# Kernel tuning notes

Hardware: AMD Instinct MI355X
Metric: run time of the kernel (lower is better)

## Reference

```python
import math
import jax, jax.numpy as jnp
import numpy as np


def _gelu(x):
    return jax.nn.gelu(x, approximate=False)


def _bilinear_sample(feat, gx, gy):
    """grid_sample, mode=bilinear, padding=border, align_corners=True.
    feat: [B,C,H,W]; gx,gy: [B,M] in [-1,1]. Returns [B,M,C]."""
    B, C, H, W = feat.shape
    x = jnp.clip((gx + 1.0) * 0.5 * (W - 1), 0.0, W - 1)
    y = jnp.clip((gy + 1.0) * 0.5 * (H - 1), 0.0, H - 1)
    x0 = jnp.floor(x); y0 = jnp.floor(y)
    wx = (x - x0)[..., None]; wy = (y - y0)[..., None]
    x0i = x0.astype(jnp.int32); y0i = y0.astype(jnp.int32)
    x1i = jnp.minimum(x0i + 1, W - 1); y1i = jnp.minimum(y0i + 1, H - 1)
    ft = jnp.transpose(feat, (0, 2, 3, 1))  # [B,H,W,C]
    gather = jax.vmap(lambda f, yi, xi: f[yi, xi])
    v00 = gather(ft, y0i, x0i); v01 = gather(ft, y0i, x1i)
    v10 = gather(ft, y1i, x0i); v11 = gather(ft, y1i, x1i)
    return (v00 * (1 - wx) * (1 - wy) + v01 * wx * (1 - wy)
            + v10 * (1 - wx) * wy + v11 * wx * wy)


def _layernorm(x, w, b, eps=1e-5):
    m = jnp.mean(x, -1, keepdims=True)
    v = jnp.var(x, -1, keepdims=True)
    return (x - m) / jnp.sqrt(v + eps) * w + b


def _gfb(h, f_next, ph_w, ph_b, gate, w1, b1, w2, b2, ln_w, ln_b):
    g = jax.nn.sigmoid(gate)
    fused = f_next + g * (h @ ph_w + ph_b)
    fused = _gelu(fused @ w1 + b1) @ w2 + b2
    return _layernorm(fused, ln_w, ln_b)


def _forward(img, feat_s8, feat_s16, coarse_flow, query_coords,
             pp_w1, pp_b1, pp_w2, pp_b2, p8_w, p8_b, p16_w, p16_b,
             f1_ph_w, f1_ph_b, f1_gate, f1_w1, f1_b1, f1_w2, f1_b2, f1_ln_w, f1_ln_b,
             f2_ph_w, f2_ph_b, f2_gate, f2_w1, f2_b1, f2_w2, f2_b2, f2_ln_w, f2_ln_b,
             h_w1, h_b1, h_w2, h_b2, h_w3, h_b3):
    B, _, H, W = img.shape
    N = query_coords.shape[1]
    k = 5; half = k // 2
    H8, W8 = coarse_flow.shape[2], coarse_flow.shape[3]
    # normalized grid at query points (x,y)
    gx = 2.0 * query_coords[..., 0] / (W - 1) - 1.0
    gy = 2.0 * query_coords[..., 1] / (H - 1) - 1.0
    coarse_q = _bilinear_sample(coarse_flow, gx, gy)  # [B,N,2]
    coarse_q = coarse_q * jnp.array([W / W8, H / H8], coarse_q.dtype)
    # local k x k RGB patches
    offs = jnp.arange(-half, half + 1, dtype=img.dtype)
    oy, ox = jnp.meshgrid(offs, offs, indexing='ij')
    og = jnp.stack([ox.reshape(-1), oy.reshape(-1)], -1)  # [k*k,2]
    ce = query_coords[:, :, None, :] + og                # [B,N,kk,2]
    pgx = (2.0 * ce[..., 0] / (W - 1) - 1.0).reshape(B, -1)
    pgy = (2.0 * ce[..., 1] / (H - 1) - 1.0).reshape(B, -1)
    patches = _bilinear_sample(img, pgx, pgy).reshape(B, N, k * k * 3)
    f_local = _gelu(patches @ pp_w1 + pp_b1) @ pp_w2 + pp_b2
    f8 = _bilinear_sample(feat_s8, gx, gy) @ p8_w + p8_b
    f16 = _bilinear_sample(feat_s16, gx, gy) @ p16_w + p16_b
    D = f_local.shape[-1]
    h = f_local.reshape(B * N, D)
    h = _gfb(h, f8.reshape(B * N, D), f1_ph_w, f1_ph_b, f1_gate,
             f1_w1, f1_b1, f1_w2, f1_b2, f1_ln_w, f1_ln_b)
    h = _gfb(h, f16.reshape(B * N, D), f2_ph_w, f2_ph_b, f2_gate,
             f2_w1, f2_b1, f2_w2, f2_b2, f2_ln_w, f2_ln_b)
    # relative-in-cell coords + sinusoidal PE (6 bands)
    qx = query_coords[..., 0] / (W / W8)
    qy = query_coords[..., 1] / (H / H8)
    local = jnp.stack([(qx - jnp.round(qx)) * 2.0, (qy - jnp.round(qy)) * 2.0], -1)
    freqs = (2.0 ** jnp.arange(6, dtype=local.dtype)) * math.pi
    xf = local[..., None] * freqs                        # [B,N,2,6]
    enc = jnp.concatenate([jnp.sin(xf), jnp.cos(xf)], -1).reshape(B, N, 24)
    pe = jnp.concatenate([local, enc], -1).reshape(B * N, 26)
    coarse_flat = coarse_q.reshape(B * N, 2)
    mi = jnp.concatenate([h, pe, coarse_flat], -1)       # [B*N, 156]
    delta = _gelu(_gelu(mi @ h_w1 + h_b1) @ h_w2 + h_b2) @ h_w3 + h_b3
    return (coarse_flat + delta).reshape(B, N, 2)


def setup_inputs() -> dict:
    key = jax.random.key(0)
    ks = jax.random.split(key, 40)
    B, H, W = 2, 384, 512
    H8, W8, H16, W16 = 48, 64, 24, 32
    N, D, k = 65536, 128, 5
    pf = 3 * k * k
    def p(i, shape):
        return jax.random.normal(ks[i], shape, jnp.float32) * 0.05
    return {
        'img': jax.random.uniform(ks[0], (B, 3, H, W), jnp.float32),
        'feat_s8': jax.random.normal(ks[1], (B, D, H8, W8), jnp.float32),
        'feat_s16': jax.random.normal(ks[2], (B, D, H16, W16), jnp.float32),
        'coarse_flow': jax.random.normal(ks[3], (B, 2, H8, W8), jnp.float32),
        'query_coords': jax.random.uniform(ks[4], (B, N, 2), jnp.float32)
                        * jnp.array([W - 1.0, H - 1.0], jnp.float32),
        'pp_w1': p(5, (pf, D)), 'pp_b1': p(6, (D,)),
        'pp_w2': p(7, (D, D)), 'pp_b2': p(8, (D,)),
        'p8_w': p(9, (D, D)), 'p8_b': p(10, (D,)),
        'p16_w': p(11, (D, D)), 'p16_b': p(12, (D,)),
        'f1_ph_w': p(13, (D, D)), 'f1_ph_b': p(14, (D,)), 'f1_gate': p(15, (D,)),
        'f1_w1': p(16, (D, 2 * D)), 'f1_b1': p(17, (2 * D,)),
        'f1_w2': p(18, (2 * D, D)), 'f1_b2': p(19, (D,)),
        'f1_ln_w': 1.0 + p(20, (D,)), 'f1_ln_b': p(21, (D,)),
        'f2_ph_w': p(22, (D, D)), 'f2_ph_b': p(23, (D,)), 'f2_gate': p(24, (D,)),
        'f2_w1': p(25, (D, 2 * D)), 'f2_b1': p(26, (2 * D,)),
        'f2_w2': p(27, (2 * D, D)), 'f2_b2': p(28, (D,)),
        'f2_ln_w': 1.0 + p(29, (D,)), 'f2_ln_b': p(30, (D,)),
        'h_w1': p(31, (D + 26 + 2, 128)), 'h_b1': p(32, (128,)),
        'h_w2': p(33, (128, 64)), 'h_b2': p(34, (64,)),
        'h_w3': p(35, (64, 2)), 'h_b3': p(36, (2,)),
    }


def reference(img, feat_s8, feat_s16, coarse_flow, query_coords,
              pp_w1, pp_b1, pp_w2, pp_b2, p8_w, p8_b, p16_w, p16_b,
              f1_ph_w, f1_ph_b, f1_gate, f1_w1, f1_b1, f1_w2, f1_b2, f1_ln_w, f1_ln_b,
              f2_ph_w, f2_ph_b, f2_gate, f2_w1, f2_b1, f2_w2, f2_b2, f2_ln_w, f2_ln_b,
              h_w1, h_b1, h_w2, h_b2, h_w3, h_b3):
    return _forward(img, feat_s8, feat_s16, coarse_flow, query_coords,
                    pp_w1, pp_b1, pp_w2, pp_b2, p8_w, p8_b, p16_w, p16_b,
                    f1_ph_w, f1_ph_b, f1_gate, f1_w1, f1_b1, f1_w2, f1_b2, f1_ln_w, f1_ln_b,
                    f2_ph_w, f2_ph_b, f2_gate, f2_w1, f2_b1, f2_w2, f2_b2, f2_ln_w, f2_ln_b,
                    h_w1, h_b1, h_w2, h_b2, h_w3, h_b3)
```

## Files before the change

kernel.cpp:

```cpp
#include <hip/hip_runtime.h>
#include <math.h>

#define NT 512
#define MB 64
#define MTOT 131072
#define IMG_H 384
#define IMG_W 512
#define H8 48
#define W8 64
#define H16 24
#define W16 32

#define SAB 136
#define SHB 168

typedef _Float16 half8_t __attribute__((ext_vector_type(8)));
typedef _Float16 half4_t __attribute__((ext_vector_type(4)));
typedef float f32x4_t __attribute__((ext_vector_type(4)));
typedef unsigned short u16;

#define PW_PP1    0
#define PW_PP2    12288
#define PW_P8CAT  28672
#define PW_P16CAT 61440
#define PW_F1W1   94208
#define PW_F1W2   126976
#define PW_F2W1   159744
#define PW_F2W2   192512
#define PW_HW1    225280
#define PW_HW2    245760
#define PW_END    253952
#define FT8_OFF   PW_END
#define FT8_CNT   (2*H8*W8*128)
#define FT16_OFF  (FT8_OFF + FT8_CNT)
#define FT16_CNT  (2*H16*W16*128)
#define FB_OFF    (FT16_OFF + FT16_CNT)

__device__ __forceinline__ u16 tohalf(float v) {
  return __builtin_bit_cast(u16, (_Float16)v);
}
__device__ __forceinline__ float geluf(float x) {
  float x2 = x * x;
  float t = x * fmaf(x2, 0.0713548162726f, 1.5957691216057308f);
  float e = __expf(-t);
  return x * __builtin_amdgcn_rcpf(1.0f + e);
}

__device__ __forceinline__ float bilin_plane(const float* __restrict__ plane,
                                             int Wd, int Hd, float x, float y) {
  x = fminf(fmaxf(x, 0.f), (float)(Wd - 1));
  y = fminf(fmaxf(y, 0.f), (float)(Hd - 1));
  float x0f = floorf(x), y0f = floorf(y);
  int x0 = (int)x0f, y0 = (int)y0f;
  int x1 = min(x0 + 1, Wd - 1), y1 = min(y0 + 1, Hd - 1);
  float wx = x - x0f, wy = y - y0f;
  const float* r0 = plane + y0 * Wd;
  const float* r1 = plane + y1 * Wd;
  float v00 = r0[x0], v01 = r0[x1], v10 = r1[x0], v11 = r1[x1];
  float top = v00 + wx * (v01 - v00);
  float bot = v10 + wx * (v11 - v10);
  return top + wy * (bot - top);
}

__device__ __forceinline__ void featSample(const u16* __restrict__ ft, int Wd, int Hd,
                                           float x, float y, u16* dstRow, int i16) {
  x = fminf(fmaxf(x, 0.f), (float)(Wd - 1));
  y = fminf(fmaxf(y, 0.f), (float)(Hd - 1));
  float x0f = floorf(x), y0f = floorf(y);
  int x0 = (int)x0f, y0 = (int)y0f;
  int x1 = min(x0 + 1, Wd - 1), y1 = min(y0 + 1, Hd - 1);
  float wx = x - x0f, wy = y - y0f;
  half8_t v00 = *reinterpret_cast<const half8_t*>(ft + (y0 * Wd + x0) * 128 + i16 * 8);
  half8_t v01 = *reinterpret_cast<const half8_t*>(ft + (y0 * Wd + x1) * 128 + i16 * 8);
  half8_t v10 = *reinterpret_cast<const half8_t*>(ft + (y1 * Wd + x0) * 128 + i16 * 8);
  half8_t v11 = *reinterpret_cast<const half8_t*>(ft + (y1 * Wd + x1) * 128 + i16 * 8);
  half8_t r;
#pragma unroll
  for (int j = 0; j < 8; ++j) {
    float top = (float)v00[j] + wx * ((float)v01[j] - (float)v00[j]);
    float bot = (float)v10[j] + wx * ((float)v11[j] - (float)v10[j]);
    r[j] = (_Float16)(top + wy * (bot - top));
  }
  *reinterpret_cast<half8_t*>(dstRow + i16 * 8) = r;
}

template <int NTW, int KT, int SPLITKT, int ACT, int NWAVES = 8>
__device__ __forceinline__ void mmv(
    const u16* __restrict__ wpk,
    const u16* aA, int strA, const u16* aB, int strB,
    const float* __restrict__ bias,
    u16* oA, int ostrA, u16* oB, int ostrB, int oSplitNt) {
  const int tid = threadIdx.x;
  const int lane = tid & 63;
  const int w = tid >> 6;
  const int l15 = lane & 15;
  const int g = lane >> 4;
  if (NWAVES == 8 || w < NWAVES) {
    f32x4_t acc[NTW][4];
#pragma unroll
    for (int i = 0; i < NTW; ++i)
#pragma unroll
      for (int mt = 0; mt < 4; ++mt) acc[i][mt] = (f32x4_t){0.f, 0.f, 0.f, 0.f};
#pragma unroll
    for (int kt = 0; kt < KT; ++kt) {
      const u16* ab = (kt < SPLITKT) ? (aA + kt * 32) : (aB + (kt - SPLITKT) * 32);
      const int str = (kt < SPLITKT) ? strA : strB;
      half8_t af[4];
#pragma unroll
      for (int mt = 0; mt < 4; ++mt)
        af[mt] = *reinterpret_cast<const half8_t*>(ab + (mt * 16 + l15) * str + g * 8);
#pragma unroll
      for (int i = 0; i < NTW; ++i) {
        const int nt = w + (i << 3);
        half8_t bf = *reinterpret_cast<const half8_t*>(wpk + ((nt * KT + kt) * 64 + lane) * 8);
#pragma unroll
        for (int mt = 0; mt < 4; ++mt)
          acc[i][mt] = __builtin_amdgcn_mfma_f32_16x16x32_f16(bf, af[mt], acc[i][mt], 0, 0, 0);
      }
    }
#pragma unroll
    for (int i = 0; i < NTW; ++i) {
      const int nt = w + (i << 3);
      const int colg = nt << 4;
      f32x4_t bv = *reinterpret_cast<const f32x4_t*>(bias + colg + (g << 2));
      u16* ob; int colB, ostr;
      if (nt < oSplitNt) { ob = oA; colB = colg; ostr = ostrA; }
      else { ob = oB; colB = colg - (oSplitNt << 4); ostr = ostrB; }
#pragma unroll
      for (int mt = 0; mt < 4; ++mt) {
        const int row = (mt << 4) + l15;
        half4_t hv;
#pragma unroll
        for (int r = 0; r < 4; ++r) {
          float v = acc[i][mt][r] + bv[r];
          if (ACT == 1) v = geluf(v);
          hv[r] = (_Float16)v;
        }
        *reinterpret_cast<half4_t*>(ob + row * ostr + colB + (g << 2)) = hv;
      }
    }
  }
}

__device__ __forceinline__ void lnorm(const u16* src, u16* dst,
                                      const float* __restrict__ lw,
                                      const float* __restrict__ lb) {
  const int tid = threadIdx.x;
  int q = tid >> 3, s = tid & 7;
  const u16* rp = src + q * SAB + s * 16;
  float xs[16];
  float sum = 0.f, sum2 = 0.f;
#pragma unroll
  for (int c8 = 0; c8 < 2; ++c8) {
    half8_t v = *reinterpret_cast<const half8_t*>(rp + c8 * 8);
#pragma unroll
    for (int j = 0; j < 8; ++j) {
      float x = (float)v[j];
      xs[c8 * 8 + j] = x; sum += x; sum2 += x * x;
    }
  }
  sum += __shfl_xor(sum, 1); sum2 += __shfl_xor(sum2, 1);
  sum += __shfl_xor(sum, 2); sum2 += __shfl_xor(sum2, 2);
  sum += __shfl_xor(sum, 4); sum2 += __shfl_xor(sum2, 4);
  float mean = sum * 0.0078125f;
  float var = sum2 * 0.0078125f - mean * mean;
  float rstd = rsqrtf(var + 1e-5f);
  u16* op = dst + q * SHB + s * 16;
#pragma unroll
  for (int c8 = 0; c8 < 2; ++c8) {
    half8_t r;
#pragma unroll
    for (int j = 0; j < 8; ++j) {
      int c = s * 16 + c8 * 8 + j;
      r[j] = (_Float16)((xs[c8 * 8 + j] - mean) * rstd * lw[c] + lb[c]);
    }
    *reinterpret_cast<half8_t*>(op + c8 * 8) = r;
  }
}

struct PackArgs {
  const float *pp_w1, *pp_w2, *p8_w, *f1_ph_w, *f1_gate, *p16_w, *f2_ph_w, *f2_gate;
  const float *f1_w1, *f1_w2, *f2_w1, *f2_w2, *h_w1, *h_w2;
  u16* dst;
};

__global__ void pack_weights(PackArgs a) {
  const int KTs[10]   = {3, 4, 8, 8, 4, 8, 4, 8, 5, 4};
  const int Ks[10]    = {75, 128, 256, 256, 128, 256, 128, 256, 156, 128};
  const int bases[11] = {0, 12288, 28672, 61440, 94208, 126976,
                         159744, 192512, 225280, 245760, 253952};
  int stride = gridDim.x * blockDim.x;
  for (int i = blockIdx.x * blockDim.x + threadIdx.x; i < PW_END; i += stride) {
    int s = 0;
    while (i >= bases[s + 1]) ++s;
    int rem = i - bases[s];
    int e = rem & 511, lane = e >> 3, j = e & 7;
    int ntkt = rem >> 9;
    int kt = ntkt % KTs[s], nt = ntkt / KTs[s];
    int k = kt * 32 + ((lane >> 4) << 3) + j;
    int col = (nt << 4) + (lane & 15);
    float v = 0.f;
    if (k < Ks[s]) {
      switch (s) {
        case 0: v = a.pp_w1[k * 128 + col]; break;
        case 1: v = a.pp_w2[k * 128 + col]; break;
        case 2: v = (k < 128) ? a.p8_w[k * 128 + col]
                              : a.f1_ph_w[(k - 128) * 128 + col] /
                                    (1.f + expf(-a.f1_gate[col])); break;
        case 3: v = (k < 128) ? a.p16_w[k * 128 + col]
                              : a.f2_ph_w[(k - 128) * 128 + col] /
                                    (1.f + expf(-a.f2_gate[col])); break;
        case 4: v = a.f1_w1[k * 256 + col]; break;
        case 5: v = a.f1_w2[k * 128 + col]; break;
        case 6: v = a.f2_w1[k * 256 + col]; break;
        case 7: v = a.f2_w2[k * 128 + col]; break;
        case 8: v = a.h_w1[k * 128 + col]; break;
        case 9: v = a.h_w2[k * 64 + col]; break;
      }
    }
    a.dst[i] = tohalf(v);
  }
}

__global__ void fuse_bias(const float* __restrict__ p8_b, const float* __restrict__ f1_ph_b,
                          const float* __restrict__ f1_gate,
                          const float* __restrict__ p16_b, const float* __restrict__ f2_ph_b,
                          const float* __restrict__ f2_gate, float* __restrict__ fb) {
  int t = threadIdx.x;
  if (t < 128) {
    fb[t] = p8_b[t] + f1_ph_b[t] / (1.f + expf(-f1_gate[t]));
    fb[128 + t] = p16_b[t] + f2_ph_b[t] / (1.f + expf(-f2_gate[t]));
  }
}

__global__ void cvt_cl_f16(const float* __restrict__ src, u16* __restrict__ dst,
                           int Hd, int Wd) {
  int total = 2 * 128 * Hd * Wd;
  int stride = gridDim.x * blockDim.x;
  for (int i = blockIdx.x * blockDim.x + threadIdx.x; i < total; i += stride) {
    int x = i % Wd;
    int t = i / Wd;
    int y = t % Hd; t /= Hd;
    int c = t % 128;
    int b = t / 128;
    dst[((b * Hd + y) * Wd + x) * 128 + c] = tohalf(src[i]);
  }
}

struct KParams {
  const float *img, *coarse_flow, *qc;
  const u16 *wpk, *ft8, *ft16;
  const float *fb;
  const float *pp_b1, *pp_b2;
  const float *f1_b1, *f1_b2, *f1_ln_w, *f1_ln_b;
  const float *f2_b1, *f2_b2, *f2_ln_w, *f2_ln_b;
  const float *h_b1, *h_b2, *h_w3, *h_b3;
  float* out;
};

__global__ __launch_bounds__(NT, 2) void ifd_mfma(KParams P) {
  __shared__ __align__(16) u16 smem[2 * (MB * SAB) + MB * SHB];
  __shared__ float qcL[2 * MB];
  __shared__ float cb[2 * MB];
  u16* ab0 = smem;
  u16* ab1 = smem + MB * SAB;
  u16* hb  = smem + 2 * MB * SAB;

  const int tid = threadIdx.x;
  const int m0 = blockIdx.x * MB;

  if (tid < 2 * MB) qcL[tid] = P.qc[m0 * 2 + tid];
  __syncthreads();

  for (int i = tid; i < MB * 96; i += NT) {
    int q = i / 96, c = i - q * 96;
    u16 val = 0;
    if (c < 75) {
      int m = m0 + q, b = m >> 16;
      float qx = qcL[2 * q], qy = qcL[2 * q + 1];
      int p = c / 3, ch = c - p * 3;
      int iy = p / 5, ix = p - iy * 5;
      const float* plane = P.img + (b * 3 + ch) * (IMG_H * IMG_W);
      val = tohalf(bilin_plane(plane, IMG_W, IMG_H,
                               qx + (float)(ix - 2), qy + (float)(iy - 2)));
    }
    ab0[q * SAB + c] = val;
  }
  for (int i = tid; i < MB * 40; i += NT) {
    int q = i / 40, c = i - q * 40;
    int m = m0 + q, b = m >> 16;
    float qx = qcL[2 * q], qy = qcL[2 * q + 1];
    float val = 0.f;
    if (c < 26) {
      float qx8 = qx * 0.125f, qy8 = qy * 0.125f;
      float lx = (qx8 - rintf(qx8)) * 2.f, ly = (qy8 - rintf(qy8)) * 2.f;
      if (c < 2) val = c ? ly : lx;
      else {
        int k = c - 2;
        int dim = k / 12, tt = k - dim * 12;
        int band = tt % 6, iscos = tt / 6;
        float loc = dim ? ly : lx;
        float ang = loc * 3.14159265358979323846f * (float)(1 << band);
        val = iscos ? __cosf(ang) : __sinf(ang);
      }
    } else if (c < 28) {
      int o = c - 26;
      float x8 = qx * (63.f / 511.f), y8 = qy * (47.f / 383.f);
      float cv = 8.f * bilin_plane(P.coarse_flow + (b * 2 + o) * (H8 * W8), W8, H8, x8, y8);
      cb[q * 2 + o] = cv;
      val = cv;
    }
    hb[q * SHB + 128 + c] = tohalf(val);
  }
  __syncthreads();

  mmv<1, 3, 3, 1>(P.wpk + PW_PP1, ab0, SAB, ab0, SAB, P.pp_b1,
                  ab1, SAB, ab1, SAB, 16);
  __syncthreads();
  mmv<1, 4, 4, 0>(P.wpk + PW_PP2, ab1, SAB, ab1, SAB, P.pp_b2,
                  hb, SHB, hb, SHB, 16);
  for (int i = tid; i < MB * 16; i += NT) {
    int q = i >> 4, i16 = i & 15;
    int m = m0 + q, b = m >> 16;
    float x = qcL[2 * q] * (63.f / 511.f), y = qcL[2 * q + 1] * (47.f / 383.f);
    featSample(P.ft8 + b * (H8 * W8 * 128), W8, H8, x, y, ab0 + q * SAB, i16);
  }
  __syncthreads();
  mmv<1, 8, 4, 0>(P.wpk + PW_P8CAT, ab0, SAB, hb, SHB, P.fb,
                  ab1, SAB, ab1, SAB, 16);
  __syncthreads();
  mmv<2, 4, 4, 1>(P.wpk + PW_F1W1, ab1, SAB, ab1, SAB, P.f1_b1,
                  ab0, SAB, hb, SHB, 8);
  __syncthreads();
  mmv<1, 8, 4, 0>(P.wpk + PW_F1W2, ab0, SAB, hb, SHB, P.f1_b2,
                  ab1, SAB, ab1, SAB, 16);
  __syncthreads();
  lnorm(ab1, hb, P.f1_ln_w, P.f1_ln_b);
  for (int i = tid; i < MB * 16; i += NT) {
    int q = i >> 4, i16 = i & 15;
    int m = m0 + q, b = m >> 16;
    float x = qcL[2 * q] * (31.f / 511.f), y = qcL[2 * q + 1] * (23.f / 383.f);
    featSample(P.ft16 + b * (H16 * W16 * 128), W16, H16, x, y, ab0 + q * SAB, i16);
  }
  __syncthreads();
  mmv<1, 8, 4, 0>(P.wpk + PW_P16CAT, ab0, SAB, hb, SHB, P.fb + 128,
                  ab1, SAB, ab1, SAB, 16);
  __syncthreads();
  mmv<2, 4, 4, 1>(P.wpk + PW_F2W1, ab1, SAB, ab1, SAB, P.f2_b1,
                  ab0, SAB, hb, SHB, 8);
  __syncthreads();
  mmv<1, 8, 4, 0>(P.wpk + PW_F2W2, ab0, SAB, hb, SHB, P.f2_b2,
                  ab1, SAB, ab1, SAB, 16);
  __syncthreads();
  lnorm(ab1, hb, P.f2_ln_w, P.f2_ln_b);
  __syncthreads();
  mmv<1, 5, 5, 1>(P.wpk + PW_HW1, hb, SHB, hb, SHB, P.h_b1,
                  ab1, SAB, ab1, SAB, 16);
  __syncthreads();
  mmv<1, 4, 4, 1, 4>(P.wpk + PW_HW2, ab1, SAB, ab1, SAB, P.h_b2,
                     ab0, SAB, ab0, SAB, 16);
  __syncthreads();
  if (tid < 2 * MB) {
    int q = tid >> 1, o = tid & 1;
    float acc = P.h_b3[o];
    const u16* rp = ab0 + q * SAB;
#pragma unroll
    for (int c8 = 0; c8 < 8; ++c8) {
      half8_t v = *reinterpret_cast<const half8_t*>(rp + c8 * 8);
#pragma unroll
      for (int j = 0; j < 8; ++j) acc += (float)v[j] * P.h_w3[(c8 * 8 + j) * 2 + o];
    }
    P.out[(m0 + q) * 2 + o] = cb[q * 2 + o] + acc;
  }
}

extern "C" void kernel_launch(void* const* d_in, const int* in_sizes, int n_in,
                              void* d_out, int out_size, void* d_ws, size_t ws_size,
                              hipStream_t stream) {
  u16* wp = (u16*)d_ws;
  float* fb = (float*)(wp + FB_OFF);

  PackArgs pa;
  pa.pp_w1  = (const float*)d_in[5];
  pa.pp_w2  = (const float*)d_in[7];
  pa.p8_w   = (const float*)d_in[9];
  pa.p16_w  = (const float*)d_in[11];
  pa.f1_ph_w = (const float*)d_in[13];
  pa.f1_gate = (const float*)d_in[15];
  pa.f1_w1  = (const float*)d_in[16];
  pa.f1_w2  = (const float*)d_in[18];
  pa.f2_ph_w = (const float*)d_in[22];
  pa.f2_gate = (const float*)d_in[24];
  pa.f2_w1  = (const float*)d_in[25];
  pa.f2_w2  = (const float*)d_in[27];
  pa.h_w1   = (const float*)d_in[31];
  pa.h_w2   = (const float*)d_in[33];
  pa.dst = wp;
  pack_weights<<<512, 256, 0, stream>>>(pa);
  fuse_bias<<<1, 128, 0, stream>>>((const float*)d_in[10], (const float*)d_in[14],
                                   (const float*)d_in[15], (const float*)d_in[12],
                                   (const float*)d_in[23], (const float*)d_in[24], fb);
  cvt_cl_f16<<<1024, 256, 0, stream>>>((const float*)d_in[1], wp + FT8_OFF, H8, W8);
  cvt_cl_f16<<<256, 256, 0, stream>>>((const float*)d_in[2], wp + FT16_OFF, H16, W16);

  KParams P;
  P.img = (const float*)d_in[0];
  P.coarse_flow = (const float*)d_in[3];
  P.qc = (const float*)d_in[4];
  P.wpk = wp; P.ft8 = wp + FT8_OFF; P.ft16 = wp + FT16_OFF;
  P.fb = fb;
  P.pp_b1 = (const float*)d_in[6];  P.pp_b2 = (const float*)d_in[8];
  P.f1_b1 = (const float*)d_in[17]; P.f1_b2 = (const float*)d_in[19];
  P.f1_ln_w = (const float*)d_in[20]; P.f1_ln_b = (const float*)d_in[21];
  P.f2_b1 = (const float*)d_in[26]; P.f2_b2 = (const float*)d_in[28];
  P.f2_ln_w = (const float*)d_in[29]; P.f2_ln_b = (const float*)d_in[30];
  P.h_b1 = (const float*)d_in[32]; P.h_b2 = (const float*)d_in[34];
  P.h_w3 = (const float*)d_in[35]; P.h_b3 = (const float*)d_in[36];
  P.out = (float*)d_out;

  ifd_mfma<<<MTOT / MB, NT, 0, stream>>>(P);
}
```

Before: 182.5 us.

## Prefetch next layer weights into registers during MFMA and raise occupancy

Each MLP layer's packed weight fragments are now loaded into registers by a callback that runs after the current layer's MFMA loop, before its epilogue, so global weight fetch latency overlaps with compute and the barrier. Launch bounds go from 2 to 4 blocks per CU, and query coordinates are read straight from global memory instead of being staged in shared memory with an extra barrier. The feature bilinear interpolation now uses packed fp16 vector math instead of fp32, which lowers precision. Holding prefetched fragments and the tighter register budget from the raised launch bound risk spills.

```diff
diff --git a/kernel.cpp b/kernel.cpp
--- a/kernel.cpp
+++ b/kernel.cpp
@@ -69,34 +69,48 @@
   float x0f = floorf(x), y0f = floorf(y);
   int x0 = (int)x0f, y0 = (int)y0f;
   int x1 = min(x0 + 1, Wd - 1), y1 = min(y0 + 1, Hd - 1);
-  float wx = x - x0f, wy = y - y0f;
+  _Float16 wx = (_Float16)(x - x0f), wy = (_Float16)(y - y0f);
   half8_t v00 = *reinterpret_cast<const half8_t*>(ft + (y0 * Wd + x0) * 128 + i16 * 8);
   half8_t v01 = *reinterpret_cast<const half8_t*>(ft + (y0 * Wd + x1) * 128 + i16 * 8);
   half8_t v10 = *reinterpret_cast<const half8_t*>(ft + (y1 * Wd + x0) * 128 + i16 * 8);
   half8_t v11 = *reinterpret_cast<const half8_t*>(ft + (y1 * Wd + x1) * 128 + i16 * 8);
-  half8_t r;
-#pragma unroll
-  for (int j = 0; j < 8; ++j) {
-    float top = (float)v00[j] + wx * ((float)v01[j] - (float)v00[j]);
-    float bot = (float)v10[j] + wx * ((float)v11[j] - (float)v10[j]);
-    r[j] = (_Float16)(top + wy * (bot - top));
-  }
+  half8_t top = v00 + wx * (v01 - v00);
+  half8_t bot = v10 + wx * (v11 - v10);
+  half8_t r = top + wy * (bot - top);
   *reinterpret_cast<half8_t*>(dstRow + i16 * 8) = r;
 }
 
-template <int NTW, int KT, int SPLITKT, int ACT, int NWAVES = 8>
+template <int NTW, int KT, int NWAVES = 8>
+__device__ __forceinline__ void wload(const u16* __restrict__ wpk, half8_t* bf) {
+  const int tid = threadIdx.x;
+  const int lane = tid & 63;
+  const int w = tid >> 6;
+  if (NWAVES == 8 || w < NWAVES) {
+#pragma unroll
+    for (int i = 0; i < NTW; ++i) {
+      const int nt = w + (i << 3);
+#pragma unroll
+      for (int kt = 0; kt < KT; ++kt)
+        bf[i * KT + kt] =
+            *reinterpret_cast<const half8_t*>(wpk + ((nt * KT + kt) * 64 + lane) * 8);
+    }
+  }
+}
+
+template <int NTW, int KT, int SPLITKT, int ACT, int NWAVES = 8, typename PF>
 __device__ __forceinline__ void mmv(
-    const u16* __restrict__ wpk,
+    const half8_t* __restrict__ bf,
     const u16* aA, int strA, const u16* aB, int strB,
     const float* __restrict__ bias,
-    u16* oA, int ostrA, u16* oB, int ostrB, int oSplitNt) {
+    u16* oA, int ostrA, u16* oB, int ostrB, int oSplitNt, PF&& pf) {
   const int tid = threadIdx.x;
   const int lane = tid & 63;
   const int w = tid >> 6;
   const int l15 = lane & 15;
   const int g = lane >> 4;
-  if (NWAVES == 8 || w < NWAVES) {
-    f32x4_t acc[NTW][4];
+  const bool active = (NWAVES == 8) || (w < NWAVES);
+  f32x4_t acc[NTW][4];
+  if (active) {
 #pragma unroll
     for (int i = 0; i < NTW; ++i)
 #pragma unroll
@@ -111,13 +125,15 @@
         af[mt] = *reinterpret_cast<const half8_t*>(ab + (mt * 16 + l15) * str + g * 8);
 #pragma unroll
       for (int i = 0; i < NTW; ++i) {
-        const int nt = w + (i << 3);
-        half8_t bf = *reinterpret_cast<const half8_t*>(wpk + ((nt * KT + kt) * 64 + lane) * 8);
 #pragma unroll
         for (int mt = 0; mt < 4; ++mt)
-          acc[i][mt] = __builtin_amdgcn_mfma_f32_16x16x32_f16(bf, af[mt], acc[i][mt], 0, 0, 0);
+          acc[i][mt] = __builtin_amdgcn_mfma_f32_16x16x32_f16(bf[i * KT + kt], af[mt],
+                                                              acc[i][mt], 0, 0, 0);
       }
     }
+  }
+  pf();
+  if (active) {
 #pragma unroll
     for (int i = 0; i < NTW; ++i) {
       const int nt = w + (i << 3);
@@ -258,9 +274,8 @@
   float* out;
 };
 
-__global__ __launch_bounds__(NT, 2) void ifd_mfma(KParams P) {
+__global__ __launch_bounds__(NT, 4) void ifd_mfma(KParams P) {
   __shared__ __align__(16) u16 smem[2 * (MB * SAB) + MB * SHB];
-  __shared__ float qcL[2 * MB];
   __shared__ float cb[2 * MB];
   u16* ab0 = smem;
   u16* ab1 = smem + MB * SAB;
@@ -269,15 +284,17 @@
   const int tid = threadIdx.x;
   const int m0 = blockIdx.x * MB;
 
-  if (tid < 2 * MB) qcL[tid] = P.qc[m0 * 2 + tid];
-  __syncthreads();
+  half8_t bS1[3], bS2[4], bS45[8], bS7[8], bS8[8], bS1112[8], bS14[8], bS15[8],
+      bS18[5], bS19[4];
+
+  wload<1, 3>(P.wpk + PW_PP1, bS1);
 
   for (int i = tid; i < MB * 96; i += NT) {
     int q = i / 96, c = i - q * 96;
     u16 val = 0;
     if (c < 75) {
       int m = m0 + q, b = m >> 16;
-      float qx = qcL[2 * q], qy = qcL[2 * q + 1];
+      float qx = P.qc[2 * m], qy = P.qc[2 * m + 1];
       int p = c / 3, ch = c - p * 3;
       int iy = p / 5, ix = p - iy * 5;
       const float* plane = P.img + (b * 3 + ch) * (IMG_H * IMG_W);
@@ -289,7 +306,7 @@
   for (int i = tid; i < MB * 40; i += NT) {
     int q = i / 40, c = i - q * 40;
     int m = m0 + q, b = m >> 16;
-    float qx = qcL[2 * q], qy = qcL[2 * q + 1];
+    float qx = P.qc[2 * m], qy = P.qc[2 * m + 1];
     float val = 0.f;
     if (c < 26) {
       float qx8 = qx * 0.125f, qy8 = qy * 0.125f;
@@ -314,51 +331,51 @@
   }
   __syncthreads();
 
-  mmv<1, 3, 3, 1>(P.wpk + PW_PP1, ab0, SAB, ab0, SAB, P.pp_b1,
-                  ab1, SAB, ab1, SAB, 16);
-  __syncthreads();
-  mmv<1, 4, 4, 0>(P.wpk + PW_PP2, ab1, SAB, ab1, SAB, P.pp_b2,
-                  hb, SHB, hb, SHB, 16);
+  mmv<1, 3, 3, 1>(bS1, ab0, SAB, ab0, SAB, P.pp_b1, ab1, SAB, ab1, SAB, 16,
+                  [&] { wload<1, 4>(P.wpk + PW_PP2, bS2); });
+  __syncthreads();
+  mmv<1, 4, 4, 0>(bS2, ab1, SAB, ab1, SAB, P.pp_b2, hb, SHB, hb, SHB, 16,
+                  [&] { wload<1, 8>(P.wpk + PW_P8CAT, bS45); });
   for (int i = tid; i < MB * 16; i += NT) {
     int q = i >> 4, i16 = i & 15;
     int m = m0 + q, b = m >> 16;
-    float x = qcL[2 * q] * (63.f / 511.f), y = qcL[2 * q + 1] * (47.f / 383.f);
+    float x = P.qc[2 * m] * (63.f / 511.f), y = P.qc[2 * m + 1] * (47.f / 383.f);
     featSample(P.ft8 + b * (H8 * W8 * 128), W8, H8, x, y, ab0 + q * SAB, i16);
   }
   __syncthreads();
-  mmv<1, 8, 4, 0>(P.wpk + PW_P8CAT, ab0, SAB, hb, SHB, P.fb,
-                  ab1, SAB, ab1, SAB, 16);
-  __syncthreads();
-  mmv<2, 4, 4, 1>(P.wpk + PW_F1W1, ab1, SAB, ab1, SAB, P.f1_b1,
-                  ab0, SAB, hb, SHB, 8);
-  __syncthreads();
-  mmv<1, 8, 4, 0>(P.wpk + PW_F1W2, ab0, SAB, hb, SHB, P.f1_b2,
-                  ab1, SAB, ab1, SAB, 16);
+  mmv<1, 8, 4, 0>(bS45, ab0, SAB, hb, SHB, P.fb, ab1, SAB, ab1, SAB, 16,
+                  [&] { wload<2, 4>(P.wpk + PW_F1W1, bS7); });
+  __syncthreads();
+  mmv<2, 4, 4, 1>(bS7, ab1, SAB, ab1, SAB, P.f1_b1, ab0, SAB, hb, SHB, 8,
+                  [&] { wload<1, 8>(P.wpk + PW_F1W2, bS8); });
+  __syncthreads();
+  mmv<1, 8, 4, 0>(bS8, ab0, SAB, hb, SHB, P.f1_b2, ab1, SAB, ab1, SAB, 16,
+                  [&] { wload<1, 8>(P.wpk + PW_P16CAT, bS1112); });
   __syncthreads();
   lnorm(ab1, hb, P.f1_ln_w, P.f1_ln_b);
   for (int i = tid; i < MB * 16; i += NT) {
     int q = i >> 4, i16 = i & 15;
     int m = m0 + q, b = m >> 16;
-    float x = qcL[2 * q] * (31.f / 511.f), y = qcL[2 * q + 1] * (23.f / 383.f);
+    float x = P.qc[2 * m] * (31.f / 511.f), y = P.qc[2 * m + 1] * (23.f / 383.f);
     featSample(P.ft16 + b * (H16 * W16 * 128), W16, H16, x, y, ab0 + q * SAB, i16);
   }
   __syncthreads();
-  mmv<1, 8, 4, 0>(P.wpk + PW_P16CAT, ab0, SAB, hb, SHB, P.fb + 128,
-                  ab1, SAB, ab1, SAB, 16);
-  __syncthreads();
-  mmv<2, 4, 4, 1>(P.wpk + PW_F2W1, ab1, SAB, ab1, SAB, P.f2_b1,
-                  ab0, SAB, hb, SHB, 8);
-  __syncthreads();
-  mmv<1, 8, 4, 0>(P.wpk + PW_F2W2, ab0, SAB, hb, SHB, P.f2_b2,
-                  ab1, SAB, ab1, SAB, 16);
+  mmv<1, 8, 4, 0>(bS1112, ab0, SAB, hb, SHB, P.fb + 128, ab1, SAB, ab1, SAB, 16,
+                  [&] { wload<2, 4>(P.wpk + PW_F2W1, bS14); });
+  __syncthreads();
+  mmv<2, 4, 4, 1>(bS14, ab1, SAB, ab1, SAB, P.f2_b1, ab0, SAB, hb, SHB, 8,
+                  [&] { wload<1, 8>(P.wpk + PW_F2W2, bS15); });
+  __syncthreads();
+  mmv<1, 8, 4, 0>(bS15, ab0, SAB, hb, SHB, P.f2_b2, ab1, SAB, ab1, SAB, 16,
+                  [&] { wload<1, 5>(P.wpk + PW_HW1, bS18); });
   __syncthreads();
   lnorm(ab1, hb, P.f2_ln_w, P.f2_ln_b);
   __syncthreads();
-  mmv<1, 5, 5, 1>(P.wpk + PW_HW1, hb, SHB, hb, SHB, P.h_b1,
-                  ab1, SAB, ab1, SAB, 16);
-  __syncthreads();
-  mmv<1, 4, 4, 1, 4>(P.wpk + PW_HW2, ab1, SAB, ab1, SAB, P.h_b2,
-                     ab0, SAB, ab0, SAB, 16);
+  mmv<1, 5, 5, 1>(bS18, hb, SHB, hb, SHB, P.h_b1, ab1, SAB, ab1, SAB, 16,
+                  [&] { wload<1, 4, 4>(P.wpk + PW_HW2, bS19); });
+  __syncthreads();
+  mmv<1, 4, 4, 1, 4>(bS19, ab1, SAB, ab1, SAB, P.h_b2, ab0, SAB, ab0, SAB, 16,
+                     [&] {});
   __syncthreads();
   if (tid < 2 * MB) {
     int q = tid >> 1, o = tid & 1;
```

Result: slower. 208.2 us (+14.1%).

## Move positional-encoding tail to global scratch and shrink LDS footprint

Applied to the files above, without the earlier changes.

The 40-column tail holding positional encodings and coarse flow moves from LDS into a per-block global scratch buffer. The hidden buffer stride shrinks and the query-coordinate and coarse-flow shared arrays are removed, which lowers LDS use per block and may allow more resident blocks. The head layer now reads its second K segment straight from global memory. The change also computes sin/cos bands with the double-angle recurrence, does the bilinear feature interpolation in packed fp16, and restructures the patch-sampling loop per thread, trading some precision and global traffic for less LDS.

```diff
diff --git a/kernel.cpp b/kernel.cpp
--- a/kernel.cpp
+++ b/kernel.cpp
@@ -12,7 +12,8 @@
 #define W16 32
 
 #define SAB 136
-#define SHB 168
+#define SHB 136
+#define SPE 40
 
 typedef _Float16 half8_t __attribute__((ext_vector_type(8)));
 typedef _Float16 half4_t __attribute__((ext_vector_type(4)));
@@ -35,6 +36,9 @@
 #define FT16_OFF  (FT8_OFF + FT8_CNT)
 #define FT16_CNT  (2*H16*W16*128)
 #define FB_OFF    (FT16_OFF + FT16_CNT)
+#define PEG_OFF   (FB_OFF + 512)
+#define PEG_CNT   (2048*MB*SPE)
+#define CBG_OFF   (PEG_OFF + PEG_CNT)
 
 __device__ __forceinline__ u16 tohalf(float v) {
   return __builtin_bit_cast(u16, (_Float16)v);
@@ -69,18 +73,14 @@
   float x0f = floorf(x), y0f = floorf(y);
   int x0 = (int)x0f, y0 = (int)y0f;
   int x1 = min(x0 + 1, Wd - 1), y1 = min(y0 + 1, Hd - 1);
-  float wx = x - x0f, wy = y - y0f;
+  _Float16 wx = (_Float16)(x - x0f), wy = (_Float16)(y - y0f);
   half8_t v00 = *reinterpret_cast<const half8_t*>(ft + (y0 * Wd + x0) * 128 + i16 * 8);
   half8_t v01 = *reinterpret_cast<const half8_t*>(ft + (y0 * Wd + x1) * 128 + i16 * 8);
   half8_t v10 = *reinterpret_cast<const half8_t*>(ft + (y1 * Wd + x0) * 128 + i16 * 8);
   half8_t v11 = *reinterpret_cast<const half8_t*>(ft + (y1 * Wd + x1) * 128 + i16 * 8);
-  half8_t r;
-#pragma unroll
-  for (int j = 0; j < 8; ++j) {
-    float top = (float)v00[j] + wx * ((float)v01[j] - (float)v00[j]);
-    float bot = (float)v10[j] + wx * ((float)v11[j] - (float)v10[j]);
-    r[j] = (_Float16)(top + wy * (bot - top));
-  }
+  half8_t top = v00 + wx * (v01 - v00);
+  half8_t bot = v10 + wx * (v11 - v10);
+  half8_t r = top + wy * (bot - top);
   *reinterpret_cast<half8_t*>(dstRow + i16 * 8) = r;
 }
 
@@ -251,6 +251,8 @@
   const float *img, *coarse_flow, *qc;
   const u16 *wpk, *ft8, *ft16;
   const float *fb;
+  u16* peg;
+  float* cbg;
   const float *pp_b1, *pp_b2;
   const float *f1_b1, *f1_b2, *f1_ln_w, *f1_ln_b;
   const float *f2_b1, *f2_b2, *f2_ln_w, *f2_ln_b;
@@ -259,58 +261,64 @@
 };
 
 __global__ __launch_bounds__(NT, 2) void ifd_mfma(KParams P) {
-  __shared__ __align__(16) u16 smem[2 * (MB * SAB) + MB * SHB];
-  __shared__ float qcL[2 * MB];
-  __shared__ float cb[2 * MB];
+  __shared__ __align__(16) u16 smem[3 * MB * SAB];
   u16* ab0 = smem;
   u16* ab1 = smem + MB * SAB;
   u16* hb  = smem + 2 * MB * SAB;
 
   const int tid = threadIdx.x;
   const int m0 = blockIdx.x * MB;
-
-  if (tid < 2 * MB) qcL[tid] = P.qc[m0 * 2 + tid];
-  __syncthreads();
-
-  for (int i = tid; i < MB * 96; i += NT) {
-    int q = i / 96, c = i - q * 96;
-    u16 val = 0;
-    if (c < 75) {
-      int m = m0 + q, b = m >> 16;
-      float qx = qcL[2 * q], qy = qcL[2 * q + 1];
-      int p = c / 3, ch = c - p * 3;
-      int iy = p / 5, ix = p - iy * 5;
-      const float* plane = P.img + (b * 3 + ch) * (IMG_H * IMG_W);
-      val = tohalf(bilin_plane(plane, IMG_W, IMG_H,
-                               qx + (float)(ix - 2), qy + (float)(iy - 2)));
-    }
-    ab0[q * SAB + c] = val;
-  }
-  for (int i = tid; i < MB * 40; i += NT) {
-    int q = i / 40, c = i - q * 40;
-    int m = m0 + q, b = m >> 16;
-    float qx = qcL[2 * q], qy = qcL[2 * q + 1];
-    float val = 0.f;
-    if (c < 26) {
-      float qx8 = qx * 0.125f, qy8 = qy * 0.125f;
-      float lx = (qx8 - rintf(qx8)) * 2.f, ly = (qy8 - rintf(qy8)) * 2.f;
-      if (c < 2) val = c ? ly : lx;
-      else {
-        int k = c - 2;
-        int dim = k / 12, tt = k - dim * 12;
-        int band = tt % 6, iscos = tt / 6;
-        float loc = dim ? ly : lx;
-        float ang = loc * 3.14159265358979323846f * (float)(1 << band);
-        val = iscos ? __cosf(ang) : __sinf(ang);
+  u16* pegB = P.peg + blockIdx.x * (MB * SPE);
+  float* cbgB = P.cbg + blockIdx.x * (MB * 2);
+
+  {
+    const int q = tid >> 3, sub = tid & 7;
+    const int m = m0 + q, b = m >> 16;
+    const float qx = P.qc[2 * m], qy = P.qc[2 * m + 1];
+    const float* imgb = P.img + b * 3 * (IMG_H * IMG_W);
+#pragma unroll
+    for (int j = 0; j < 12; ++j) {
+      const int c = sub * 12 + j;
+      u16 val = 0;
+      if (c < 75) {
+        int p = c / 3, ch = c - p * 3;
+        int iy = p / 5, ix = p - iy * 5;
+        val = tohalf(bilin_plane(imgb + ch * (IMG_H * IMG_W), IMG_W, IMG_H,
+                                 qx + (float)(ix - 2), qy + (float)(iy - 2)));
       }
-    } else if (c < 28) {
-      int o = c - 26;
-      float x8 = qx * (63.f / 511.f), y8 = qy * (47.f / 383.f);
-      float cv = 8.f * bilin_plane(P.coarse_flow + (b * 2 + o) * (H8 * W8), W8, H8, x8, y8);
-      cb[q * 2 + o] = cv;
-      val = cv;
-    }
-    hb[q * SHB + 128 + c] = tohalf(val);
+      ab0[q * SAB + c] = val;
+    }
+  }
+  if (tid < 128) {
+    const int q = tid >> 1, dim = tid & 1;
+    const int m = m0 + q;
+    const float qv = P.qc[2 * m + dim];
+    const float q8 = qv * 0.125f;
+    const float loc = (q8 - rintf(q8)) * 2.f;
+    pegB[q * SPE + dim] = tohalf(loc);
+    const float th = loc * 3.14159265358979323846f;
+    float s = __sinf(th), c = __cosf(th);
+    const int base = q * SPE + 2 + dim * 12;
+#pragma unroll
+    for (int bnd = 0; bnd < 6; ++bnd) {
+      pegB[base + bnd] = tohalf(s);
+      pegB[base + 6 + bnd] = tohalf(c);
+      float s2 = 2.f * s * c;
+      c = fmaf(-2.f * s, s, 1.f);
+      s = s2;
+    }
+  } else if (tid < 256) {
+    const int t2 = tid - 128, q = t2 >> 1, o = t2 & 1;
+    const int m = m0 + q, b = m >> 16;
+    const float qx = P.qc[2 * m], qy = P.qc[2 * m + 1];
+    const float x8 = qx * (63.f / 511.f), y8 = qy * (47.f / 383.f);
+    const float cv = 8.f * bilin_plane(P.coarse_flow + (b * 2 + o) * (H8 * W8),
+                                       W8, H8, x8, y8);
+    pegB[q * SPE + 26 + o] = tohalf(cv);
+    cbgB[q * 2 + o] = cv;
+  } else if (tid < 384) {
+    const int t2 = tid - 256, q = t2 >> 1, pr = t2 & 1;
+    *reinterpret_cast<unsigned int*>(pegB + q * SPE + 28 + 2 * pr) = 0u;
   }
   __syncthreads();
 
@@ -322,7 +330,7 @@
   for (int i = tid; i < MB * 16; i += NT) {
     int q = i >> 4, i16 = i & 15;
     int m = m0 + q, b = m >> 16;
-    float x = qcL[2 * q] * (63.f / 511.f), y = qcL[2 * q + 1] * (47.f / 383.f);
+    float x = P.qc[2 * m] * (63.f / 511.f), y = P.qc[2 * m + 1] * (47.f / 383.f);
     featSample(P.ft8 + b * (H8 * W8 * 128), W8, H8, x, y, ab0 + q * SAB, i16);
   }
   __syncthreads();
@@ -339,7 +347,7 @@
   for (int i = tid; i < MB * 16; i += NT) {
     int q = i >> 4, i16 = i & 15;
     int m = m0 + q, b = m >> 16;
-    float x = qcL[2 * q] * (31.f / 511.f), y = qcL[2 * q + 1] * (23.f / 383.f);
+    float x = P.qc[2 * m] * (31.f / 511.f), y = P.qc[2 * m + 1] * (23.f / 383.f);
     featSample(P.ft16 + b * (H16 * W16 * 128), W16, H16, x, y, ab0 + q * SAB, i16);
   }
   __syncthreads();
@@ -354,7 +362,7 @@
   __syncthreads();
   lnorm(ab1, hb, P.f2_ln_w, P.f2_ln_b);
   __syncthreads();
-  mmv<1, 5, 5, 1>(P.wpk + PW_HW1, hb, SHB, hb, SHB, P.h_b1,
+  mmv<1, 5, 4, 1>(P.wpk + PW_HW1, hb, SHB, pegB, SPE, P.h_b1,
                   ab1, SAB, ab1, SAB, 16);
   __syncthreads();
   mmv<1, 4, 4, 1, 4>(P.wpk + PW_HW2, ab1, SAB, ab1, SAB, P.h_b2,
@@ -370,7 +378,7 @@
 #pragma unroll
       for (int j = 0; j < 8; ++j) acc += (float)v[j] * P.h_w3[(c8 * 8 + j) * 2 + o];
     }
-    P.out[(m0 + q) * 2 + o] = cb[q * 2 + o] + acc;
+    P.out[(m0 + q) * 2 + o] = cbgB[q * 2 + o] + acc;
   }
 }
 
@@ -379,6 +387,8 @@
                               hipStream_t stream) {
   u16* wp = (u16*)d_ws;
   float* fb = (float*)(wp + FB_OFF);
+  u16* peg = wp + PEG_OFF;
+  float* cbg = (float*)(wp + CBG_OFF);
 
   PackArgs pa;
   pa.pp_w1  = (const float*)d_in[5];
@@ -408,7 +418,7 @@
   P.coarse_flow = (const float*)d_in[3];
   P.qc = (const float*)d_in[4];
   P.wpk = wp; P.ft8 = wp + FT8_OFF; P.ft16 = wp + FT16_OFF;
-  P.fb = fb;
+  P.fb = fb; P.peg = peg; P.cbg = cbg;
   P.pp_b1 = (const float*)d_in[6];  P.pp_b2 = (const float*)d_in[8];
   P.f1_b1 = (const float*)d_in[17]; P.f1_b2 = (const float*)d_in[19];
   P.f1_ln_w = (const float*)d_in[20]; P.f1_ln_b = (const float*)d_in[21];
```

Result: no change. 184.6 us (+1.2%).
